# Performance work log

Hardware: AMD Instinct MI355X
Metric: run time of the kernel (lower is better)

Reference implementation:

```python
import jax, jax.numpy as jnp
import numpy as np

B, L, D, H = 2, 2048, 1024, 16
P = D // H  # head dim = 64


def setup_inputs() -> dict:
    key = jax.random.key(0)
    ks = jax.random.split(key, 9)
    s = 1.0 / np.sqrt(D)
    x = jax.random.normal(ks[0], (B, L, D), dtype=jnp.float32)
    Wq = jax.random.normal(ks[1], (D, D), dtype=jnp.float32) * s
    bq = jax.random.normal(ks[2], (D,), dtype=jnp.float32) * 0.02
    Wk = jax.random.normal(ks[3], (D, D), dtype=jnp.float32) * s
    bk = jax.random.normal(ks[4], (D,), dtype=jnp.float32) * 0.02
    Wv = jax.random.normal(ks[5], (D, D), dtype=jnp.float32) * s
    bv = jax.random.normal(ks[6], (D,), dtype=jnp.float32) * 0.02
    Wo = jax.random.normal(ks[7], (D, D), dtype=jnp.float32) * s
    bo = jax.random.normal(ks[8], (D,), dtype=jnp.float32) * 0.02
    return {"token_activations": x, "Wq": Wq, "bq": bq, "Wk": Wk, "bk": bk,
            "Wv": Wv, "bv": bv, "Wo": Wo, "bo": bo}


def _split_heads(t):
    # 'b l (h p) -> b h l p'
    b, l, d = t.shape
    return t.reshape(b, l, H, P).transpose(0, 2, 1, 3)


def reference(token_activations, Wq, bq, Wk, bk, Wv, bv, Wo, bo):
    x = token_activations
    q = _split_heads(x @ Wq.T + bq)  # [B,H,L,P]
    k = _split_heads(x @ Wk.T + bk)
    v = _split_heads(x @ Wv.T + bv)
    # pattern[b,h,l,m] = K_l . Q_m / sqrt(P)
    scores = jnp.einsum('bhlp,bhmp->bhlm', k, q) / jnp.sqrt(jnp.float32(P))
    attn = jax.nn.softmax(scores, axis=-2)  # softmax over key axis l
    # out at query position m: sum_l attn[l,m] * V_l
    o = jnp.einsum('bhlm,bhlp->bhmp', attn, v)  # [B,H,L,P] (m indexed)
    o = o.transpose(0, 2, 1, 3).reshape(x.shape[0], x.shape[1], D)  # 'b h m p -> b m (h p)'
    return o @ Wo.T + bo
```

## Files before the change

### kernel.cpp

```cpp
#include <hip/hip_runtime.h>

typedef unsigned short u16;
typedef float f32x4 __attribute__((ext_vector_type(4)));
typedef __bf16 bf16x8 __attribute__((ext_vector_type(8)));
typedef __bf16 bf16x4 __attribute__((ext_vector_type(4)));

#define DEV static __device__ __forceinline__

constexpr int kB = 2;
constexpr int kL = 2048;
constexpr int kD = 1024;
constexpr int kH = 16;
constexpr int kP = 64;
constexpr int kM = kB * kL;
constexpr float kQScale = 0.125f * 1.44269504088896f;

DEV u16 f2bf(float x) {
  union { float f; unsigned u; } v;
  v.f = x;
  unsigned r = v.u + 0x7fffu + ((v.u >> 16) & 1u);
  return (u16)(r >> 16);
}

DEV void gload16(const void* g, void* l) {
  __builtin_amdgcn_global_load_lds(
      (const __attribute__((address_space(1))) unsigned int*)g,
      (__attribute__((address_space(3))) unsigned int*)l, 16, 0, 0);
}

__global__ void cvt_kernel(const float* __restrict__ src, u16* __restrict__ dst, int n4) {
  int i = blockIdx.x * blockDim.x + threadIdx.x;
  if (i >= n4) return;
  float4 v = reinterpret_cast<const float4*>(src)[i];
  uint2 o;
  o.x = (unsigned)f2bf(v.x) | ((unsigned)f2bf(v.y) << 16);
  o.y = (unsigned)f2bf(v.z) | ((unsigned)f2bf(v.w) << 16);
  reinterpret_cast<uint2*>(dst)[i] = o;
}

__global__ void cvtw_kernel(const float* __restrict__ w0, const float* __restrict__ w1,
                            const float* __restrict__ w2, const float* __restrict__ w3,
                            u16* __restrict__ o0, u16* __restrict__ o1,
                            u16* __restrict__ o2, u16* __restrict__ o3) {
  int sel = blockIdx.x >> 10;
  int i = (blockIdx.x & 1023) * 256 + threadIdx.x;
  const float* src = sel == 0 ? w0 : (sel == 1 ? w1 : (sel == 2 ? w2 : w3));
  u16* dst = sel == 0 ? o0 : (sel == 1 ? o1 : (sel == 2 ? o2 : o3));
  float4 v = reinterpret_cast<const float4*>(src)[i];
  uint2 o;
  o.x = (unsigned)f2bf(v.x) | ((unsigned)f2bf(v.y) << 16);
  o.y = (unsigned)f2bf(v.z) | ((unsigned)f2bf(v.w) << 16);
  reinterpret_cast<uint2*>(dst)[i] = o;
}

template <bool SWAP>
DEV void gemm_core(const u16* __restrict__ A, const u16* __restrict__ W,
                   int m0, int n0, u16* As, u16* Bs, f32x4 acc[4][4]) {
  const int tid = threadIdx.x;
  const int w = tid >> 6, lane = tid & 63;
  const int wr = w >> 1, wc = w & 1;
  const int g = lane >> 4, c = lane & 15;
  const int srow = lane >> 2;
  const int skoff = (lane & 3) * 8;

  const u16* ga0 = A + (size_t)(m0 + w * 32 + srow) * kD + skoff;
  const u16* ga1 = ga0 + (size_t)16 * kD;
  const u16* gb0 = W + (size_t)(n0 + w * 32 + srow) * kD + skoff;
  const u16* gb1 = gb0 + (size_t)16 * kD;
  u16* Ad0 = As + (w * 32) * 32;
  u16* Ad1 = As + (w * 32 + 16) * 32;
  u16* Bd0 = Bs + (w * 32) * 32;
  u16* Bd1 = Bs + (w * 32 + 16) * 32;

  auto stage = [&](int buf) {
    gload16(ga0, Ad0 + buf * 4096);
    gload16(ga1, Ad1 + buf * 4096);
    gload16(gb0, Bd0 + buf * 4096);
    gload16(gb1, Bd1 + buf * 4096);
    ga0 += 32; ga1 += 32; gb0 += 32; gb1 += 32;
  };

  auto compute = [&](int buf) {
    const u16* Ab = As + buf * 4096;
    const u16* Bb = Bs + buf * 4096;
    bf16x8 af[4], bfr[4];
#pragma unroll
    for (int f = 0; f < 4; ++f) {
      af[f]  = *reinterpret_cast<const bf16x8*>(Ab + (wr * 64 + f * 16 + c) * 32 + g * 8);
      bfr[f] = *reinterpret_cast<const bf16x8*>(Bb + (wc * 64 + f * 16 + c) * 32 + g * 8);
    }
    __builtin_amdgcn_s_setprio(1);
#pragma unroll
    for (int fi = 0; fi < 4; ++fi)
#pragma unroll
      for (int fj = 0; fj < 4; ++fj) {
        if constexpr (SWAP)
          acc[fj][fi] = __builtin_amdgcn_mfma_f32_16x16x32_bf16(bfr[fj], af[fi], acc[fj][fi], 0, 0, 0);
        else
          acc[fi][fj] = __builtin_amdgcn_mfma_f32_16x16x32_bf16(af[fi], bfr[fj], acc[fi][fj], 0, 0, 0);
      }
    __builtin_amdgcn_s_setprio(0);
  };

  stage(0);
  __syncthreads();
  for (int k0 = 0; k0 < kD; k0 += 64) {
    stage(1);
    compute(0);
    __syncthreads();
    if (k0 + 64 < kD) stage(0);
    compute(1);
    __syncthreads();
  }
}

__global__ __launch_bounds__(256) void qkv_kernel(
    const u16* __restrict__ xb,
    const u16* __restrict__ wq, const u16* __restrict__ wk, const u16* __restrict__ wv,
    const float* __restrict__ bq, const float* __restrict__ bk, const float* __restrict__ bv,
    u16* __restrict__ qb, u16* __restrict__ kb, u16* __restrict__ vtb) {
  __shared__ u16 As[2 * 128 * 32], Bs[2 * 128 * 32];
  const int mb = blockIdx.x, nb = blockIdx.y;
  const int sel = nb >> 3;
  const int m0 = mb * 128, n0 = (nb & 7) * 128;
  const u16* W = sel == 0 ? wq : (sel == 1 ? wk : wv);
  const float* bias = sel == 0 ? bq : (sel == 1 ? bk : bv);

  const int lane = threadIdx.x & 63, w = threadIdx.x >> 6;
  const int wr = w >> 1, wc = w & 1, g = lane >> 4, c = lane & 15;
  const int bb = m0 >> 11;
  const int lbase = (m0 & 2047) + wr * 64;

  f32x4 acc[4][4];
#pragma unroll
  for (int i = 0; i < 4; ++i)
#pragma unroll
    for (int j = 0; j < 4; ++j) acc[i][j] = f32x4{0.f, 0.f, 0.f, 0.f};

  if (sel < 2) {
    gemm_core<true>(xb, W, m0, n0, As, Bs, acc);
    u16* dst = sel == 0 ? qb : kb;
    const float scale = (sel == 0) ? kQScale : 1.0f;
#pragma unroll
    for (int fj = 0; fj < 4; ++fj) {
      const int n4 = n0 + wc * 64 + fj * 16 + g * 4;
      const float4 b4 = *reinterpret_cast<const float4*>(&bias[n4]);
      const int hh = n4 >> 6, p0 = n4 & 63;
      u16* base = dst + ((size_t)(bb * kH + hh)) * kL * kP + p0;
#pragma unroll
      for (int fi = 0; fi < 4; ++fi) {
        const int l = lbase + fi * 16 + c;
        bf16x4 o;
        o[0] = (__bf16)((acc[fj][fi][0] + b4.x) * scale);
        o[1] = (__bf16)((acc[fj][fi][1] + b4.y) * scale);
        o[2] = (__bf16)((acc[fj][fi][2] + b4.z) * scale);
        o[3] = (__bf16)((acc[fj][fi][3] + b4.w) * scale);
        *reinterpret_cast<bf16x4*>(base + (size_t)l * kP) = o;
      }
    }
  } else {
    gemm_core<false>(xb, W, m0, n0, As, Bs, acc);
#pragma unroll
    for (int fj = 0; fj < 4; ++fj) {
      const int n = n0 + wc * 64 + fj * 16 + c;
      const float bv_ = bias[n];
      const int hh = n >> 6, p = n & 63;
      u16* base = vtb + (((size_t)(bb * kH + hh)) * kP + p) * kL;
#pragma unroll
      for (int fi = 0; fi < 4; ++fi) {
        const int l4 = lbase + fi * 16 + g * 4;
        bf16x4 o;
#pragma unroll
        for (int r = 0; r < 4; ++r) o[r] = (__bf16)(acc[fi][fj][r] + bv_);
        *reinterpret_cast<bf16x4*>(base + l4) = o;
      }
    }
  }
}

__global__ __launch_bounds__(256) void out_kernel(
    const u16* __restrict__ ob, const u16* __restrict__ wo,
    const float* __restrict__ bo, float* __restrict__ out) {
  __shared__ u16 As[2 * 128 * 32], Bs[2 * 128 * 32];
  const int m0 = blockIdx.x * 128, n0 = blockIdx.y * 128;
  f32x4 acc[4][4];
#pragma unroll
  for (int i = 0; i < 4; ++i)
#pragma unroll
    for (int j = 0; j < 4; ++j) acc[i][j] = f32x4{0.f, 0.f, 0.f, 0.f};

  gemm_core<true>(ob, wo, m0, n0, As, Bs, acc);

  const int lane = threadIdx.x & 63, w = threadIdx.x >> 6;
  const int wr = w >> 1, wc = w & 1, g = lane >> 4, c = lane & 15;
#pragma unroll
  for (int fj = 0; fj < 4; ++fj) {
    const int n4 = n0 + wc * 64 + fj * 16 + g * 4;
    const float4 b4 = *reinterpret_cast<const float4*>(&bo[n4]);
#pragma unroll
    for (int fi = 0; fi < 4; ++fi) {
      const int m = m0 + wr * 64 + fi * 16 + c;
      float4 o;
      o.x = acc[fj][fi][0] + b4.x;
      o.y = acc[fj][fi][1] + b4.y;
      o.z = acc[fj][fi][2] + b4.z;
      o.w = acc[fj][fi][3] + b4.w;
      *reinterpret_cast<float4*>(&out[(size_t)m * kD + n4]) = o;
    }
  }
}

__global__ __launch_bounds__(512, 2) void attn_kernel(
    const u16* __restrict__ qb, const u16* __restrict__ kb,
    const u16* __restrict__ vtb, u16* __restrict__ ob) {
  __shared__ __align__(16) char kvs[2][2][8192];
  __shared__ __align__(16) char pts[8][2048];
  const int tid = threadIdx.x, w = tid >> 6, lane = tid & 63;
  const int g = lane >> 4, c = lane & 15;
  const int h = blockIdx.y, b = blockIdx.z;
  const size_t hoff = ((size_t)(b * kH + h)) * kL * kP;
  const char* Qg = (const char*)(qb + hoff);
  const char* Kg = (const char*)(kb + hoff);
  const char* Vg = (const char*)(vtb + hoff);
  const int q0 = blockIdx.x * 128 + w * 16;

  const int lrow = lane >> 3;
  const int spb = ((lane & 7) ^ lrow) << 4;
  const char* kp = Kg + (size_t)(w * 8 + lrow) * 128 + spb;
  const char* vp = Vg + (size_t)(w * 8 + lrow) * (kL * 2) + spb;

  auto stage = [&](int buf) {
    gload16(kp, &kvs[buf][0][w * 1024]);
    gload16(vp, &kvs[buf][1][w * 1024]);
    kp += 64 * 128;
    vp += 128;
  };

  const int csw = (c & 7) << 4;
  const int kvb0 = c * 128 + ((g * 16) ^ csw);
  const int kvb1 = c * 128 + ((64 + g * 16) ^ csw);
  char* myPt = &pts[w][0];

  bf16x8 qf[2];
#pragma unroll
  for (int kc = 0; kc < 2; ++kc)
    qf[kc] = *reinterpret_cast<const bf16x8*>(Qg + (size_t)(q0 + c) * 128 + kc * 64 + g * 16);

  f32x4 oacc[4];
#pragma unroll
  for (int pt = 0; pt < 4; ++pt) oacc[pt] = f32x4{0.f, 0.f, 0.f, 0.f};
  float Srun = 0.f;

  stage(0);
  __syncthreads();

  constexpr int NT = kL / 64;
  auto body = [&](int cur, int t) {
    if (t + 1 < NT) stage(cur ^ 1);
    const char* Ks = &kvs[cur][0][0];
    const char* Vs = &kvs[cur][1][0];

    f32x4 s[4];
    __builtin_amdgcn_s_setprio(1);
#pragma unroll
    for (int lt = 0; lt < 4; ++lt) {
      bf16x8 k0 = *reinterpret_cast<const bf16x8*>(Ks + lt * 2048 + kvb0);
      bf16x8 k1 = *reinterpret_cast<const bf16x8*>(Ks + lt * 2048 + kvb1);
      f32x4 z = f32x4{0.f, 0.f, 0.f, 0.f};
      z = __builtin_amdgcn_mfma_f32_16x16x32_bf16(k0, qf[0], z, 0, 0, 0);
      z = __builtin_amdgcn_mfma_f32_16x16x32_bf16(k1, qf[1], z, 0, 0, 0);
      s[lt] = z;
    }
    __builtin_amdgcn_s_setprio(0);

    float tsum = 0.f;
#pragma unroll
    for (int lt = 0; lt < 4; ++lt) {
      bf16x4 pv;
#pragma unroll
      for (int r = 0; r < 4; ++r) {
        float p = __builtin_amdgcn_exp2f(s[lt][r]);
        tsum += p;
        pv[r] = (__bf16)p;
      }
      *reinterpret_cast<bf16x4*>(myPt + c * 128 + ((lt * 32 + g * 8) ^ csw)) = pv;
    }
    Srun += tsum;

    bf16x8 pf0 = *reinterpret_cast<const bf16x8*>(myPt + kvb0);
    bf16x8 pf1 = *reinterpret_cast<const bf16x8*>(myPt + kvb1);
    __builtin_amdgcn_s_setprio(1);
#pragma unroll
    for (int pt = 0; pt < 4; ++pt) {
      bf16x8 v0 = *reinterpret_cast<const bf16x8*>(Vs + pt * 2048 + kvb0);
      bf16x8 v1 = *reinterpret_cast<const bf16x8*>(Vs + pt * 2048 + kvb1);
      oacc[pt] = __builtin_amdgcn_mfma_f32_16x16x32_bf16(pf0, v0, oacc[pt], 0, 0, 0);
      oacc[pt] = __builtin_amdgcn_mfma_f32_16x16x32_bf16(pf1, v1, oacc[pt], 0, 0, 0);
    }
    __builtin_amdgcn_s_setprio(0);
    __syncthreads();
  };

  for (int t = 0; t < NT; t += 2) {
    body(0, t);
    body(1, t + 1);
  }

  Srun += __shfl_xor(Srun, 16, 64);
  Srun += __shfl_xor(Srun, 32, 64);

  float rs = 1.f / Srun;
  float fr[4];
#pragma unroll
  for (int r = 0; r < 4; ++r) fr[r] = __shfl(rs, g * 4 + r, 64);
#pragma unroll
  for (int pt = 0; pt < 4; ++pt)
#pragma unroll
    for (int r = 0; r < 4; ++r) {
      int q = q0 + g * 4 + r;
      ob[((size_t)(b * kL + q)) * kD + h * kP + pt * 16 + c] = f2bf(oacc[pt][r] * fr[r]);
    }
}

extern "C" void kernel_launch(void* const* d_in, const int* in_sizes, int n_in,
                              void* d_out, int out_size, void* d_ws, size_t ws_size,
                              hipStream_t stream) {
  (void)in_sizes; (void)n_in; (void)out_size; (void)ws_size;
  const float* x  = (const float*)d_in[0];
  const float* Wq = (const float*)d_in[1];
  const float* bq = (const float*)d_in[2];
  const float* Wk = (const float*)d_in[3];
  const float* bk = (const float*)d_in[4];
  const float* Wv = (const float*)d_in[5];
  const float* bv = (const float*)d_in[6];
  const float* Wo = (const float*)d_in[7];
  const float* bo = (const float*)d_in[8];
  float* out = (float*)d_out;

  char* ws = (char*)d_ws;
  u16* xb  = (u16*)(ws);
  u16* wqb = (u16*)(ws + (8u << 20));
  u16* wkb = (u16*)(ws + (10u << 20));
  u16* wvb = (u16*)(ws + (12u << 20));
  u16* wob = (u16*)(ws + (14u << 20));
  u16* qb  = (u16*)(ws + (16u << 20));
  u16* kb  = (u16*)(ws + (24u << 20));
  u16* vtb = (u16*)(ws + (32u << 20));

  cvt_kernel<<<kM * kD / 1024, 256, 0, stream>>>(x, xb, kM * kD / 4);
  cvtw_kernel<<<4096, 256, 0, stream>>>(Wq, Wk, Wv, Wo, wqb, wkb, wvb, wob);

  qkv_kernel<<<dim3(kM / 128, 24), 256, 0, stream>>>(
      xb, wqb, wkb, wvb, bq, bk, bv, qb, kb, vtb);

  attn_kernel<<<dim3(kL / 128, kH, kB), 512, 0, stream>>>(qb, kb, vtb, xb);

  out_kernel<<<dim3(kM / 128, kD / 128), 256, 0, stream>>>(xb, wob, bo, out);
}
```

Measured before the change: 134.1 us.

## Replace double-buffered GEMM staging with single-buffer XOR-swizzled LDS tiles

Rewrites the shared projection GEMM core so each K-step loads one 32-wide tile into a single LDS buffer, computes on it, and syncs twice per step. The double buffer and the s_setprio hints are dropped. An XOR swizzle on the 16-byte chunk offsets is added to cut LDS bank conflicts on fragment reads. Halving LDS use may allow more resident blocks, but global-load latency is no longer overlapped with MFMA work and barriers per K element double.

```diff
diff --git a/kernel.cpp b/kernel.cpp
--- a/kernel.cpp
+++ b/kernel.cpp
@@ -54,42 +54,33 @@
 }
 
 template <bool SWAP>
-DEV void gemm_core(const u16* __restrict__ A, const u16* __restrict__ W,
+DEV void gemm_tile(const u16* __restrict__ A, const u16* __restrict__ W,
                    int m0, int n0, u16* As, u16* Bs, f32x4 acc[4][4]) {
   const int tid = threadIdx.x;
   const int w = tid >> 6, lane = tid & 63;
   const int wr = w >> 1, wc = w & 1;
   const int g = lane >> 4, c = lane & 15;
   const int srow = lane >> 2;
-  const int skoff = (lane & 3) * 8;
-
-  const u16* ga0 = A + (size_t)(m0 + w * 32 + srow) * kD + skoff;
-  const u16* ga1 = ga0 + (size_t)16 * kD;
-  const u16* gb0 = W + (size_t)(n0 + w * 32 + srow) * kD + skoff;
-  const u16* gb1 = gb0 + (size_t)16 * kD;
-  u16* Ad0 = As + (w * 32) * 32;
-  u16* Ad1 = As + (w * 32 + 16) * 32;
-  u16* Bd0 = Bs + (w * 32) * 32;
-  u16* Bd1 = Bs + (w * 32 + 16) * 32;
-
-  auto stage = [&](int buf) {
-    gload16(ga0, Ad0 + buf * 4096);
-    gload16(ga1, Ad1 + buf * 4096);
-    gload16(gb0, Bd0 + buf * 4096);
-    gload16(gb1, Bd1 + buf * 4096);
-    ga0 += 32; ga1 += 32; gb0 += 32; gb1 += 32;
-  };
-
-  auto compute = [&](int buf) {
-    const u16* Ab = As + buf * 4096;
-    const u16* Bb = Bs + buf * 4096;
+  const int skoff = ((lane & 3) ^ (srow & 3)) * 8;
+  const int rsl0 = (g ^ (c & 3)) * 8;
+
+  for (int k0 = 0; k0 < kD; k0 += 32) {
+    __syncthreads();
+#pragma unroll
+    for (int j = 0; j < 2; ++j) {
+      const u16* ga = A + (size_t)(m0 + w * 32 + j * 16 + srow) * kD + k0 + skoff;
+      gload16(ga, As + (w * 32 + j * 16) * 32);
+      const u16* gb = W + (size_t)(n0 + w * 32 + j * 16 + srow) * kD + k0 + skoff;
+      gload16(gb, Bs + (w * 32 + j * 16) * 32);
+    }
+    __syncthreads();
+
     bf16x8 af[4], bfr[4];
 #pragma unroll
     for (int f = 0; f < 4; ++f) {
-      af[f]  = *reinterpret_cast<const bf16x8*>(Ab + (wr * 64 + f * 16 + c) * 32 + g * 8);
-      bfr[f] = *reinterpret_cast<const bf16x8*>(Bb + (wc * 64 + f * 16 + c) * 32 + g * 8);
-    }
-    __builtin_amdgcn_s_setprio(1);
+      af[f]  = *reinterpret_cast<const bf16x8*>(As + (wr * 64 + f * 16 + c) * 32 + rsl0);
+      bfr[f] = *reinterpret_cast<const bf16x8*>(Bs + (wc * 64 + f * 16 + c) * 32 + rsl0);
+    }
 #pragma unroll
     for (int fi = 0; fi < 4; ++fi)
 #pragma unroll
@@ -99,18 +90,6 @@
         else
           acc[fi][fj] = __builtin_amdgcn_mfma_f32_16x16x32_bf16(af[fi], bfr[fj], acc[fi][fj], 0, 0, 0);
       }
-    __builtin_amdgcn_s_setprio(0);
-  };
-
-  stage(0);
-  __syncthreads();
-  for (int k0 = 0; k0 < kD; k0 += 64) {
-    stage(1);
-    compute(0);
-    __syncthreads();
-    if (k0 + 64 < kD) stage(0);
-    compute(1);
-    __syncthreads();
   }
 }
 
@@ -119,7 +98,7 @@
     const u16* __restrict__ wq, const u16* __restrict__ wk, const u16* __restrict__ wv,
     const float* __restrict__ bq, const float* __restrict__ bk, const float* __restrict__ bv,
     u16* __restrict__ qb, u16* __restrict__ kb, u16* __restrict__ vtb) {
-  __shared__ u16 As[2 * 128 * 32], Bs[2 * 128 * 32];
+  __shared__ u16 As[128 * 32], Bs[128 * 32];
   const int mb = blockIdx.x, nb = blockIdx.y;
   const int sel = nb >> 3;
   const int m0 = mb * 128, n0 = (nb & 7) * 128;
@@ -138,7 +117,7 @@
     for (int j = 0; j < 4; ++j) acc[i][j] = f32x4{0.f, 0.f, 0.f, 0.f};
 
   if (sel < 2) {
-    gemm_core<true>(xb, W, m0, n0, As, Bs, acc);
+    gemm_tile<true>(xb, W, m0, n0, As, Bs, acc);
     u16* dst = sel == 0 ? qb : kb;
     const float scale = (sel == 0) ? kQScale : 1.0f;
 #pragma unroll
@@ -159,7 +138,7 @@
       }
     }
   } else {
-    gemm_core<false>(xb, W, m0, n0, As, Bs, acc);
+    gemm_tile<false>(xb, W, m0, n0, As, Bs, acc);
 #pragma unroll
     for (int fj = 0; fj < 4; ++fj) {
       const int n = n0 + wc * 64 + fj * 16 + c;
@@ -181,7 +160,7 @@
 __global__ __launch_bounds__(256) void out_kernel(
     const u16* __restrict__ ob, const u16* __restrict__ wo,
     const float* __restrict__ bo, float* __restrict__ out) {
-  __shared__ u16 As[2 * 128 * 32], Bs[2 * 128 * 32];
+  __shared__ u16 As[128 * 32], Bs[128 * 32];
   const int m0 = blockIdx.x * 128, n0 = blockIdx.y * 128;
   f32x4 acc[4][4];
 #pragma unroll
@@ -189,7 +168,7 @@
 #pragma unroll
     for (int j = 0; j < 4; ++j) acc[i][j] = f32x4{0.f, 0.f, 0.f, 0.f};
 
-  gemm_core<true>(ob, wo, m0, n0, As, Bs, acc);
+  gemm_tile<true>(ob, wo, m0, n0, As, Bs, acc);
 
   const int lane = threadIdx.x & 63, w = threadIdx.x >> 6;
   const int wr = w >> 1, wc = w & 1, g = lane >> 4, c = lane & 15;
```

Result: faster. 117.6 us (-12.3%).
